# Kernel tuning notes

Measured on AMD Instinct MI355X. Metric: run time of the kernel, lower is better.

Reference implementation:

```python
import jax, jax.numpy as jnp
import numpy as np


def _hilbert_envelope(x1d):
    """|analytic signal| of a real 1-D signal, matching scipy.signal.hilbert."""
    N = x1d.shape[0]  # static at trace time
    h = np.zeros(N, dtype=np.float32)
    if N % 2 == 0:
        h[0] = 1.0
        h[N // 2] = 1.0
        h[1:N // 2] = 2.0
    else:
        h[0] = 1.0
        h[1:(N + 1) // 2] = 2.0
    Xf = jnp.fft.fft(x1d)
    analytic = jnp.fft.ifft(Xf * jnp.asarray(h))
    return jnp.abs(analytic)


def setup_inputs() -> dict:
    key = jax.random.key(0)
    B, L, D = 32, 4096, 64
    x = jax.random.normal(key, (B, L, D), dtype=jnp.float32)
    return {"x": x}


def reference(x):
    B, L, D = x.shape
    flat = x.reshape(-1)  # [B*L*D], one long signal as in the original
    up = jnp.clip(flat, 0.0, None)
    down = jnp.clip(-flat, 0.0, None)
    envelope_max = _hilbert_envelope(up).reshape(B, L, D)
    envelope_min = (-_hilbert_envelope(down)).reshape(B, L, D)
    avg_envelope = (envelope_max + envelope_min) * 0.5
    imf = x - avg_envelope
    # torch.std(dim=1, unbiased=True) -> ddof=1 over the time axis
    std_res = jnp.std(imf, axis=1, keepdims=True, ddof=1) + jnp.float32(0.01)
    return imf / std_res, avg_envelope
```

## Files before the change

kernel.cpp:

```cpp
#include <hip/hip_runtime.h>
#include <math.h>

#define NTOT 8388608
#define N1   2048
#define N2   4096
#define BB   32
#define LL   4096
#define DD   64

enum { M_NONE = 0, M_TW = 1, M_SCALE = 4 };

__device__ inline float2 cmul(float2 a, float2 b) {
    return make_float2(a.x*b.x - a.y*b.y, a.x*b.y + a.y*b.x);
}
__device__ inline float2 cadd(float2 a, float2 b){ return make_float2(a.x+b.x, a.y+b.y); }
__device__ inline float2 csub(float2 a, float2 b){ return make_float2(a.x-b.x, a.y-b.y); }
__device__ inline float2 mul_pi(float2 a){ return make_float2(-a.y, a.x); }
__device__ inline float2 mul_mi(float2 a){ return make_float2(a.y, -a.x); }
__device__ inline int pidx(int a){ return a + (a >> 3); }

template<bool INV>
__device__ inline void dft8(const float2* x, float2* y) {
    const float C = 0.70710678118654752f;
    float2 t0=cadd(x[0],x[4]), t1=cadd(x[1],x[5]), t2=cadd(x[2],x[6]), t3=cadd(x[3],x[7]);
    float2 u0=csub(x[0],x[4]), u1=csub(x[1],x[5]), u2=csub(x[2],x[6]), u3=csub(x[3],x[7]);
    if (!INV) {
        u1 = make_float2(C*(u1.x+u1.y), C*(u1.y-u1.x));
        u2 = mul_mi(u2);
        u3 = make_float2(C*(u3.y-u3.x), -C*(u3.x+u3.y));
    } else {
        u1 = make_float2(C*(u1.x-u1.y), C*(u1.y+u1.x));
        u2 = mul_pi(u2);
        u3 = make_float2(-C*(u3.x+u3.y), C*(u3.x-u3.y));
    }
    {
        float2 s0=cadd(t0,t2), s1=cadd(t1,t3), d0=csub(t0,t2);
        float2 d1 = INV ? mul_pi(csub(t1,t3)) : mul_mi(csub(t1,t3));
        y[0]=cadd(s0,s1); y[4]=csub(s0,s1); y[2]=cadd(d0,d1); y[6]=csub(d0,d1);
    }
    {
        float2 s0=cadd(u0,u2), s1=cadd(u1,u3), d0=csub(u0,u2);
        float2 d1 = INV ? mul_pi(csub(u1,u3)) : mul_mi(csub(u1,u3));
        y[1]=cadd(s0,s1); y[5]=csub(s0,s1); y[3]=cadd(d0,d1); y[7]=csub(d0,d1);
    }
}

template<bool INV>
__device__ inline void dft4(const float2* u, float2* y) {
    float2 s0=cadd(u[0],u[2]), s1=cadd(u[1],u[3]), d0=csub(u[0],u[2]);
    float2 d1 = INV ? mul_pi(csub(u[1],u[3])) : mul_mi(csub(u[1],u[3]));
    y[0]=cadd(s0,s1); y[2]=csub(s0,s1); y[1]=cadd(d0,d1); y[3]=csub(d0,d1);
}

template<bool INV, int SH>
__device__ inline void twiddle8(float2* y, int ps, const float2* __restrict__ T1t) {
    #pragma unroll
    for (int k = 1; k < 8; ++k) {
        int idx = ((ps * k) << SH) & 4095;
        float2 w = T1t[idx];
        if (INV) w.y = -w.y;
        y[k] = cmul(y[k], w);
    }
}

__global__ __launch_bounds__(256) void gen_tables(float2* T1, float2* T2) {
    int j = blockIdx.x * 256 + threadIdx.x;
    if (j < 4096) {
        double ang = -2.0 * M_PI * (double)j / 4096.0;
        T1[j] = make_float2((float)cos(ang), (float)sin(ang));
    } else if (j < 4096 + 2048) {
        int b = j - 4096;
        double ang = -2.0 * M_PI * (double)b / 8388608.0;
        T2[b] = make_float2((float)cos(ang), (float)sin(ang));
    }
}

template<bool INV, int MODE>
__global__ __launch_bounds__(512) void fft4096(float2* data,
                                               const float2* __restrict__ T1t,
                                               const float2* __restrict__ T2t) {
    __shared__ float SR[4608];
    __shared__ float SI[4608];
    const int t = threadIdx.x;
    const int r = blockIdx.x;
    float2* base = data + (size_t)r * 4096;

    float2 x[8], y[8];
    #pragma unroll
    for (int m = 0; m < 8; ++m) x[m] = base[t + 512*m];

    #pragma unroll
    for (int st = 0; st < 3; ++st) {
        const int s = 1 << (3*st);
        const int q = t & (s - 1);
        const int ps = t - q;
        dft8<INV>(x, y);
        twiddle8<INV, 0>(y, ps, T1t);
        if (st) __syncthreads();
        #pragma unroll
        for (int k = 0; k < 8; ++k) {
            int a = 8*ps + q + k*s;
            SR[pidx(a)] = y[k].x; SI[pidx(a)] = y[k].y;
        }
        __syncthreads();
        #pragma unroll
        for (int m = 0; m < 8; ++m) {
            int a = t + 512*m;
            x[m] = make_float2(SR[pidx(a)], SI[pidx(a)]);
        }
    }
    dft8<INV>(x, y);
    #pragma unroll
    for (int k = 0; k < 8; ++k) {
        int o = t + 512*k;
        float2 v = y[k];
        if (MODE == M_TW) {
            int tt = r * o;
            float2 w = cmul(T1t[tt >> 11], T2t[tt & 2047]);
            if (INV) w.y = -w.y;
            v = cmul(v, w);
        } else if (MODE == M_SCALE) {
            const float sc = 1.f / 8388608.f;
            v.x *= sc; v.y *= sc;
        }
        base[o] = v;
    }
}

__global__ __launch_bounds__(256) void fftmid(float2* data,
                                              const float2* __restrict__ T1t,
                                              const float2* __restrict__ T2t) {
    __shared__ float SR[2304];
    __shared__ float SI[2304];
    const int t = threadIdx.x;
    const int r = blockIdx.x;
    float2* base = data + (size_t)r * 2048;

    float2 x[8], y[8];
    #pragma unroll
    for (int m = 0; m < 8; ++m) x[m] = base[t + 256*m];

    #pragma unroll
    for (int st = 0; st < 3; ++st) {
        const int s = 1 << (3*st);
        const int q = t & (s - 1);
        const int ps = t - q;
        dft8<false>(x, y);
        twiddle8<false, 1>(y, ps, T1t);
        if (st) __syncthreads();
        #pragma unroll
        for (int k = 0; k < 8; ++k) {
            int a = 8*ps + q + k*s;
            SR[pidx(a)] = y[k].x; SI[pidx(a)] = y[k].y;
        }
        __syncthreads();
        if (st < 2) {
            #pragma unroll
            for (int m = 0; m < 8; ++m) {
                int a = t + 256*m;
                x[m] = make_float2(SR[pidx(a)], SI[pidx(a)]);
            }
        }
    }
    float2 xa[4], xb[4], ya[4], yb[4];
    #pragma unroll
    for (int m = 0; m < 4; ++m) {
        int a = t + 512*m;        xa[m] = make_float2(SR[pidx(a)], SI[pidx(a)]);
        int b = t + 256 + 512*m;  xb[m] = make_float2(SR[pidx(b)], SI[pidx(b)]);
    }
    dft4<false>(xa, ya);
    dft4<false>(xb, yb);
    __syncthreads();
    #pragma unroll
    for (int k = 0; k < 4; ++k) {
        int o = t + 512*k;
        float h = (o < 1024) ? ((o == 0 && r == 0) ? 1.f : 2.f)
                             : ((o == 1024 && r == 0) ? 1.f : 0.f);
        SR[pidx(o)] = ya[k].x * h; SI[pidx(o)] = ya[k].y * h;
        int o2 = o + 256;
        float h2 = (o2 < 1024) ? 2.f : 0.f;
        SR[pidx(o2)] = yb[k].x * h2; SI[pidx(o2)] = yb[k].y * h2;
    }
    __syncthreads();
    #pragma unroll
    for (int m = 0; m < 8; ++m) {
        int a = t + 256*m;
        x[m] = make_float2(SR[pidx(a)], SI[pidx(a)]);
    }
    #pragma unroll
    for (int st = 0; st < 3; ++st) {
        const int s = 1 << (3*st);
        const int q = t & (s - 1);
        const int ps = t - q;
        dft8<true>(x, y);
        twiddle8<true, 1>(y, ps, T1t);
        __syncthreads();
        #pragma unroll
        for (int k = 0; k < 8; ++k) {
            int a = 8*ps + q + k*s;
            SR[pidx(a)] = y[k].x; SI[pidx(a)] = y[k].y;
        }
        __syncthreads();
        if (st < 2) {
            #pragma unroll
            for (int m = 0; m < 8; ++m) {
                int a = t + 256*m;
                x[m] = make_float2(SR[pidx(a)], SI[pidx(a)]);
            }
        }
    }
    #pragma unroll
    for (int m = 0; m < 4; ++m) {
        int a = t + 512*m;        xa[m] = make_float2(SR[pidx(a)], SI[pidx(a)]);
        int b = t + 256 + 512*m;  xb[m] = make_float2(SR[pidx(b)], SI[pidx(b)]);
    }
    dft4<true>(xa, ya);
    dft4<true>(xb, yb);
    #pragma unroll
    for (int k = 0; k < 4; ++k) {
        int o = t + 512*k;
        int tt = r * o;
        float2 w = cmul(T1t[tt >> 11], T2t[tt & 2047]);
        w.y = -w.y;
        base[o] = cmul(ya[k], w);
        int o2 = o + 256;
        int tt2 = r * o2;
        float2 w2 = cmul(T1t[tt2 >> 11], T2t[tt2 & 2047]);
        w2.y = -w2.y;
        base[o2] = cmul(yb[k], w2);
    }
}

__global__ __launch_bounds__(256) void k_pre(const float* __restrict__ x, float2* __restrict__ A) {
    __shared__ float tile[32][33];
    int c0 = blockIdx.x * 32;
    int r0 = blockIdx.y * 32;
    int tx = threadIdx.x, ty = threadIdx.y;
    #pragma unroll
    for (int j = 0; j < 32; j += 8)
        tile[ty + j][tx] = x[(size_t)(r0 + ty + j) * N1 + c0 + tx];
    __syncthreads();
    #pragma unroll
    for (int j = 0; j < 32; j += 8) {
        float v = tile[tx][ty + j];
        A[(size_t)(c0 + ty + j) * N2 + r0 + tx] = make_float2(fmaxf(v, 0.f), fmaxf(-v, 0.f));
    }
}

__global__ __launch_bounds__(256) void k_trans(const float2* __restrict__ in, float2* __restrict__ out,
                                               int inCols, int inRows) {
    __shared__ float2 tile[32][33];
    int c0 = blockIdx.x * 32;
    int r0 = blockIdx.y * 32;
    int tx = threadIdx.x, ty = threadIdx.y;
    #pragma unroll
    for (int j = 0; j < 32; j += 8)
        tile[ty + j][tx] = in[(size_t)(r0 + ty + j) * inCols + c0 + tx];
    __syncthreads();
    #pragma unroll
    for (int j = 0; j < 32; j += 8)
        out[(size_t)(c0 + ty + j) * inRows + r0 + tx] = tile[tx][ty + j];
}

__global__ __launch_bounds__(256) void k_post(const float2* __restrict__ A, const float* __restrict__ x,
                                              float* __restrict__ out) {
    __shared__ float2 tile[32][33];
    int c0 = blockIdx.x * 32;
    int r0 = blockIdx.y * 32;
    int tx = threadIdx.x, ty = threadIdx.y;
    #pragma unroll
    for (int j = 0; j < 32; j += 8)
        tile[ty + j][tx] = A[(size_t)(r0 + ty + j) * N2 + c0 + tx];
    __syncthreads();
    #pragma unroll
    for (int j = 0; j < 32; j += 8) {
        int n2 = c0 + ty + j;
        int n1 = r0 + tx;
        size_t n = (size_t)n2 * N1 + n1;
        float2 w = tile[tx][ty + j];
        float xv = x[n];
        float up = fmaxf(xv, 0.f);
        float dn = fmaxf(-xv, 0.f);
        float hu = w.y - dn;
        float hd = up - w.x;
        float em = sqrtf(up*up + hu*hu);
        float en = sqrtf(dn*dn + hd*hd);
        float avg = 0.5f * (em - en);
        out[n]        = xv - avg;
        out[NTOT + n] = avg;
    }
}

__global__ __launch_bounds__(256) void std_partial(const float* __restrict__ imf, float* __restrict__ part) {
    int blk = blockIdx.x;
    int b   = blk >> 4;
    int ch  = blk & 15;
    int d   = threadIdx.x & 63;
    int lw  = threadIdx.x >> 6;
    float s1 = 0.f, s2 = 0.f;
    const float* base = imf + (size_t)b * LL * DD;
    for (int i = 0; i < 64; ++i) {
        int l = ch * 256 + lw * 64 + i;
        float v = base[(size_t)l * DD + d];
        s1 += v;
        s2 += v * v;
    }
    __shared__ float r1[4][64];
    __shared__ float r2[4][64];
    r1[lw][d] = s1; r2[lw][d] = s2;
    __syncthreads();
    if (lw == 0) {
        s1 = r1[0][d] + r1[1][d] + r1[2][d] + r1[3][d];
        s2 = r2[0][d] + r2[1][d] + r2[2][d] + r2[3][d];
        int pi = blk * 64 + d;
        part[pi] = s1;
        part[BB * 16 * 64 + pi] = s2;
    }
}

__global__ __launch_bounds__(256) void std_final(const float* __restrict__ part, float* __restrict__ scalev) {
    int g = blockIdx.x * 256 + threadIdx.x;
    int b = g >> 6, d = g & 63;
    float s1 = 0.f, s2 = 0.f;
    for (int ch = 0; ch < 16; ++ch) {
        int pi = (b * 16 + ch) * 64 + d;
        s1 += part[pi];
        s2 += part[BB * 16 * 64 + pi];
    }
    float mean = s1 / (float)LL;
    float var  = (s2 - (float)LL * mean * mean) / (float)(LL - 1);
    var = fmaxf(var, 0.f);
    scalev[g] = 1.f / (sqrtf(var) + 0.01f);
}

__global__ __launch_bounds__(256) void apply_scale(float* __restrict__ out, const float* __restrict__ scalev) {
    size_t i = ((size_t)blockIdx.x * 256 + threadIdx.x) * 4;
    float4 v = *(float4*)(out + i);
    int b = (int)(i >> 18);
    int d = (int)(i & 63);
    const float* sc = scalev + b * 64;
    v.x *= sc[d];
    v.y *= sc[d + 1];
    v.z *= sc[d + 2];
    v.w *= sc[d + 3];
    *(float4*)(out + i) = v;
}

extern "C" void kernel_launch(void* const* d_in, const int* in_sizes, int n_in,
                              void* d_out, int out_size, void* d_ws, size_t ws_size,
                              hipStream_t stream) {
    const float* x = (const float*)d_in[0];
    float* out = (float*)d_out;
    char* w = (char*)d_ws;

    float2* T1     = (float2*)w;
    float2* T2     = (float2*)(w + 32 * 1024);
    float*  part   = (float*)(w + 48 * 1024);
    float*  scalev = (float*)(w + 320 * 1024);
    float2* A      = (float2*)(w + (1 << 20));
    float2* Bbuf   = (float2*)d_out;

    hipLaunchKernelGGL(gen_tables, dim3(24), dim3(256), 0, stream, T1, T2);

    hipLaunchKernelGGL(k_pre, dim3(N1/32, N2/32), dim3(32, 8), 0, stream, x, A);
    hipLaunchKernelGGL((fft4096<false, M_TW>), dim3(N1), dim3(512), 0, stream, A, T1, T2);
    hipLaunchKernelGGL(k_trans, dim3(N2/32, N1/32), dim3(32, 8), 0, stream, A, Bbuf, N2, N1);
    hipLaunchKernelGGL(fftmid, dim3(N2), dim3(256), 0, stream, Bbuf, T1, T2);
    hipLaunchKernelGGL(k_trans, dim3(N1/32, N2/32), dim3(32, 8), 0, stream, Bbuf, A, N1, N2);
    hipLaunchKernelGGL((fft4096<true, M_SCALE>), dim3(N1), dim3(512), 0, stream, A, T1, T2);
    hipLaunchKernelGGL(k_post, dim3(N2/32, N1/32), dim3(32, 8), 0, stream, A, x, out);

    hipLaunchKernelGGL(std_partial, dim3(BB * 16), dim3(256), 0, stream, out, part);
    hipLaunchKernelGGL(std_final, dim3(8), dim3(256), 0, stream, part, scalev);
    hipLaunchKernelGGL(apply_scale, dim3(NTOT / 4 / 256), dim3(256), 0, stream, out, scalev);
}
```

Before: 233.9 us.

## Use interleaved float2 LDS, exploit zeroed spectrum half in inverse mid FFT

Shared memory moves from split real/imag float arrays to a single padded float2 array, so each element needs one LDS access instead of two, with padding changed to one slot per 16 elements. In fftmid, the Hilbert mask zeroes the upper half of the spectrum, so the first inverse radix-8 stage reads only four nonzero inputs through a specialized dft8, with the Nyquist term at index 1024 added by thread 0. Conjugate twiddle multiplies are fused into a cmul_conj helper. The first-stage special case adds a divergent branch on thread 0 and relies on the half-zero structure being exact.

```diff
diff --git a/kernel.cpp b/kernel.cpp
--- a/kernel.cpp
+++ b/kernel.cpp
@@ -13,11 +13,14 @@
 __device__ inline float2 cmul(float2 a, float2 b) {
     return make_float2(a.x*b.x - a.y*b.y, a.x*b.y + a.y*b.x);
 }
+__device__ inline float2 cmul_conj(float2 a, float2 b) {
+    return make_float2(a.x*b.x + a.y*b.y, a.y*b.x - a.x*b.y);
+}
 __device__ inline float2 cadd(float2 a, float2 b){ return make_float2(a.x+b.x, a.y+b.y); }
 __device__ inline float2 csub(float2 a, float2 b){ return make_float2(a.x-b.x, a.y-b.y); }
 __device__ inline float2 mul_pi(float2 a){ return make_float2(-a.y, a.x); }
 __device__ inline float2 mul_mi(float2 a){ return make_float2(a.y, -a.x); }
-__device__ inline int pidx(int a){ return a + (a >> 3); }
+__device__ inline int pidx(int a){ return a + (a >> 4); }
 
 template<bool INV>
 __device__ inline void dft8(const float2* x, float2* y) {
@@ -45,6 +48,23 @@
     }
 }
 
+__device__ inline void dft8_h0_inv(const float2* x, float2* y) {
+    const float C = 0.70710678118654752f;
+    float2 u1 = make_float2(C*(x[1].x - x[1].y), C*(x[1].y + x[1].x));
+    float2 u2 = mul_pi(x[2]);
+    float2 u3 = make_float2(-C*(x[3].x + x[3].y), C*(x[3].x - x[3].y));
+    {
+        float2 s0=cadd(x[0],x[2]), s1=cadd(x[1],x[3]), d0=csub(x[0],x[2]);
+        float2 d1 = mul_pi(csub(x[1],x[3]));
+        y[0]=cadd(s0,s1); y[4]=csub(s0,s1); y[2]=cadd(d0,d1); y[6]=csub(d0,d1);
+    }
+    {
+        float2 s0=cadd(x[0],u2), s1=cadd(u1,u3), d0=csub(x[0],u2);
+        float2 d1 = mul_pi(csub(u1,u3));
+        y[1]=cadd(s0,s1); y[5]=csub(s0,s1); y[3]=cadd(d0,d1); y[7]=csub(d0,d1);
+    }
+}
+
 template<bool INV>
 __device__ inline void dft4(const float2* u, float2* y) {
     float2 s0=cadd(u[0],u[2]), s1=cadd(u[1],u[3]), d0=csub(u[0],u[2]);
@@ -58,8 +78,7 @@
     for (int k = 1; k < 8; ++k) {
         int idx = ((ps * k) << SH) & 4095;
         float2 w = T1t[idx];
-        if (INV) w.y = -w.y;
-        y[k] = cmul(y[k], w);
+        y[k] = INV ? cmul_conj(y[k], w) : cmul(y[k], w);
     }
 }
 
@@ -79,8 +98,7 @@
 __global__ __launch_bounds__(512) void fft4096(float2* data,
                                                const float2* __restrict__ T1t,
                                                const float2* __restrict__ T2t) {
-    __shared__ float SR[4608];
-    __shared__ float SI[4608];
+    __shared__ float2 S[4352];
     const int t = threadIdx.x;
     const int r = blockIdx.x;
     float2* base = data + (size_t)r * 4096;
@@ -98,16 +116,10 @@
         twiddle8<INV, 0>(y, ps, T1t);
         if (st) __syncthreads();
         #pragma unroll
-        for (int k = 0; k < 8; ++k) {
-            int a = 8*ps + q + k*s;
-            SR[pidx(a)] = y[k].x; SI[pidx(a)] = y[k].y;
-        }
+        for (int k = 0; k < 8; ++k) S[pidx(8*ps + q + k*s)] = y[k];
         __syncthreads();
         #pragma unroll
-        for (int m = 0; m < 8; ++m) {
-            int a = t + 512*m;
-            x[m] = make_float2(SR[pidx(a)], SI[pidx(a)]);
-        }
+        for (int m = 0; m < 8; ++m) x[m] = S[pidx(t + 512*m)];
     }
     dft8<INV>(x, y);
     #pragma unroll
@@ -117,8 +129,7 @@
         if (MODE == M_TW) {
             int tt = r * o;
             float2 w = cmul(T1t[tt >> 11], T2t[tt & 2047]);
-            if (INV) w.y = -w.y;
-            v = cmul(v, w);
+            v = INV ? cmul_conj(v, w) : cmul(v, w);
         } else if (MODE == M_SCALE) {
             const float sc = 1.f / 8388608.f;
             v.x *= sc; v.y *= sc;
@@ -130,8 +141,7 @@
 __global__ __launch_bounds__(256) void fftmid(float2* data,
                                               const float2* __restrict__ T1t,
                                               const float2* __restrict__ T2t) {
-    __shared__ float SR[2304];
-    __shared__ float SI[2304];
+    __shared__ float2 S[2176];
     const int t = threadIdx.x;
     const int r = blockIdx.x;
     float2* base = data + (size_t)r * 2048;
@@ -149,24 +159,18 @@
         twiddle8<false, 1>(y, ps, T1t);
         if (st) __syncthreads();
         #pragma unroll
-        for (int k = 0; k < 8; ++k) {
-            int a = 8*ps + q + k*s;
-            SR[pidx(a)] = y[k].x; SI[pidx(a)] = y[k].y;
-        }
+        for (int k = 0; k < 8; ++k) S[pidx(8*ps + q + k*s)] = y[k];
         __syncthreads();
         if (st < 2) {
             #pragma unroll
-            for (int m = 0; m < 8; ++m) {
-                int a = t + 256*m;
-                x[m] = make_float2(SR[pidx(a)], SI[pidx(a)]);
-            }
+            for (int m = 0; m < 8; ++m) x[m] = S[pidx(t + 256*m)];
         }
     }
     float2 xa[4], xb[4], ya[4], yb[4];
     #pragma unroll
     for (int m = 0; m < 4; ++m) {
-        int a = t + 512*m;        xa[m] = make_float2(SR[pidx(a)], SI[pidx(a)]);
-        int b = t + 256 + 512*m;  xb[m] = make_float2(SR[pidx(b)], SI[pidx(b)]);
+        xa[m] = S[pidx(t + 512*m)];
+        xb[m] = S[pidx(t + 256 + 512*m)];
     }
     dft4<false>(xa, ya);
     dft4<false>(xb, yb);
@@ -174,45 +178,50 @@
     #pragma unroll
     for (int k = 0; k < 4; ++k) {
         int o = t + 512*k;
-        float h = (o < 1024) ? ((o == 0 && r == 0) ? 1.f : 2.f)
-                             : ((o == 1024 && r == 0) ? 1.f : 0.f);
-        SR[pidx(o)] = ya[k].x * h; SI[pidx(o)] = ya[k].y * h;
+        if (o < 1024) {
+            float h = (o == 0 && r == 0) ? 1.f : 2.f;
+            S[pidx(o)] = make_float2(ya[k].x * h, ya[k].y * h);
+        } else if (o == 1024) {
+            S[pidx(1024)] = (r == 0) ? ya[k] : make_float2(0.f, 0.f);
+        }
         int o2 = o + 256;
-        float h2 = (o2 < 1024) ? 2.f : 0.f;
-        SR[pidx(o2)] = yb[k].x * h2; SI[pidx(o2)] = yb[k].y * h2;
-    }
-    __syncthreads();
-    #pragma unroll
-    for (int m = 0; m < 8; ++m) {
-        int a = t + 256*m;
-        x[m] = make_float2(SR[pidx(a)], SI[pidx(a)]);
-    }
-    #pragma unroll
-    for (int st = 0; st < 3; ++st) {
+        if (o2 < 1024) S[pidx(o2)] = make_float2(yb[k].x * 2.f, yb[k].y * 2.f);
+    }
+    __syncthreads();
+    #pragma unroll
+    for (int m = 0; m < 4; ++m) x[m] = S[pidx(t + 256*m)];
+    dft8_h0_inv(x, y);
+    if (t == 0) {
+        float2 c = S[pidx(1024)];
+        #pragma unroll
+        for (int k = 0; k < 8; ++k) {
+            if (k & 1) { y[k].x -= c.x; y[k].y -= c.y; }
+            else       { y[k].x += c.x; y[k].y += c.y; }
+        }
+    }
+    twiddle8<true, 1>(y, t, T1t);
+    __syncthreads();
+    #pragma unroll
+    for (int k = 0; k < 8; ++k) S[pidx(8*t + k)] = y[k];
+    __syncthreads();
+    #pragma unroll
+    for (int st = 1; st < 3; ++st) {
         const int s = 1 << (3*st);
         const int q = t & (s - 1);
         const int ps = t - q;
+        #pragma unroll
+        for (int m = 0; m < 8; ++m) x[m] = S[pidx(t + 256*m)];
         dft8<true>(x, y);
         twiddle8<true, 1>(y, ps, T1t);
         __syncthreads();
         #pragma unroll
-        for (int k = 0; k < 8; ++k) {
-            int a = 8*ps + q + k*s;
-            SR[pidx(a)] = y[k].x; SI[pidx(a)] = y[k].y;
-        }
+        for (int k = 0; k < 8; ++k) S[pidx(8*ps + q + k*s)] = y[k];
         __syncthreads();
-        if (st < 2) {
-            #pragma unroll
-            for (int m = 0; m < 8; ++m) {
-                int a = t + 256*m;
-                x[m] = make_float2(SR[pidx(a)], SI[pidx(a)]);
-            }
-        }
     }
     #pragma unroll
     for (int m = 0; m < 4; ++m) {
-        int a = t + 512*m;        xa[m] = make_float2(SR[pidx(a)], SI[pidx(a)]);
-        int b = t + 256 + 512*m;  xb[m] = make_float2(SR[pidx(b)], SI[pidx(b)]);
+        xa[m] = S[pidx(t + 512*m)];
+        xb[m] = S[pidx(t + 256 + 512*m)];
     }
     dft4<true>(xa, ya);
     dft4<true>(xb, yb);
@@ -221,13 +230,11 @@
         int o = t + 512*k;
         int tt = r * o;
         float2 w = cmul(T1t[tt >> 11], T2t[tt & 2047]);
-        w.y = -w.y;
-        base[o] = cmul(ya[k], w);
+        base[o] = cmul_conj(ya[k], w);
         int o2 = o + 256;
         int tt2 = r * o2;
         float2 w2 = cmul(T1t[tt2 >> 11], T2t[tt2 & 2047]);
-        w2.y = -w2.y;
-        base[o2] = cmul(yb[k], w2);
+        base[o2] = cmul_conj(yb[k], w2);
     }
 }
 
```

Result: no change. 231.6 us (-1.0%).
